# Kernel optimization log

Hardware: AMD Instinct MI355X
Metric: run time of the kernel (lower is better)

## Reference

```python
import jax, jax.numpy as jnp
import numpy as np

WINDOW = 8  # outlier_fraction = 0.125 -> 1 fp column kept per 8-wide window

# XnorBinaryLinear's STEBinary: sign in fwd, identity (straight-through) in bwd
@jax.custom_vjp
def ste_sign(x):
    return jnp.sign(x)

def _ste_fwd(x):
    return jnp.sign(x), None

def _ste_bwd(_, g):
    return (g,)

ste_sign.defvjp(_ste_fwd, _ste_bwd)


def quant_weight(w):
    # XnorBinaryLinear.quant_weight: per-row mean-center, sign, rescale by
    # detached per-row mean absolute value
    mu = jnp.mean(w, axis=-1, keepdims=True)
    wc = w - mu
    scale = jax.lax.stop_gradient(jnp.mean(jnp.abs(wc), axis=-1, keepdims=True))
    return ste_sign(wc) * scale


def binarize_except_outliers(w):
    # Binarize weight, then restore the max-|w| element of each flat 8-wide
    # window to full precision (calibration = argmax of |w| per window,
    # identical to outlier_calibration with L1 metric on first forward).
    wq = quant_weight(w)
    wv = w.reshape(-1, WINDOW)             # [n_windows, 8]
    idx = jnp.argmax(jnp.abs(wv), axis=1)  # [n_windows] outlier column per window
    mask = jnp.arange(WINDOW)[None, :] == idx[:, None]  # one-hot bool mask
    out = jnp.where(mask, wv, wq.reshape(-1, WINDOW))
    return out.reshape(w.shape)


def setup_inputs() -> dict:
    key = jax.random.key(0)
    k1, k2, k3 = jax.random.split(key, 3)
    x = jax.random.normal(k1, (4, 2048, 4096), dtype=jnp.float32)
    weight = jax.random.normal(k2, (4096, 4096), dtype=jnp.float32) * 0.02
    bias = jax.random.normal(k3, (4096,), dtype=jnp.float32) * 0.02
    return {"x": x, "weight": weight, "bias": bias}


def reference(x, weight, bias):
    w = binarize_except_outliers(weight)     # [OC, IC]
    return jnp.einsum('bsi,oi->bso', x, w) + bias
```

## Files before the change

kernel.cpp:

```cpp
#include <hip/hip_runtime.h>
#include <stdint.h>

#define M_DIM 8192
#define N_DIM 4096
#define K_DIM 4096

#define BM 128
#define BN 256
#define BK 64

typedef float v16f __attribute__((ext_vector_type(16)));
typedef __bf16 v8bf __attribute__((ext_vector_type(8)));

typedef __attribute__((address_space(3))) uint32_t lds_u32_t;
typedef const __attribute__((address_space(1))) uint32_t glb_u32_t;

__device__ inline uint16_t f2bf(float f) {
    union { float f; uint32_t u; } v; v.f = f;
    uint32_t r = v.u + 0x7fffu + ((v.u >> 16) & 1u);
    return (uint16_t)(r >> 16);
}

__global__ __launch_bounds__(256) void cvt_x(const float* __restrict__ x,
                                             uint16_t* __restrict__ xb,
                                             long long n8) {
    long long i = (long long)blockIdx.x * 256 + threadIdx.x;
    if (i >= n8) return;
    const float4* x4 = (const float4*)x;
    float4 a = x4[2 * i];
    float4 b = x4[2 * i + 1];
    union { uint16_t h[8]; uint4 u; } o;
    o.h[0] = f2bf(a.x); o.h[1] = f2bf(a.y); o.h[2] = f2bf(a.z); o.h[3] = f2bf(a.w);
    o.h[4] = f2bf(b.x); o.h[5] = f2bf(b.y); o.h[6] = f2bf(b.z); o.h[7] = f2bf(b.w);
    ((uint4*)xb)[i] = o.u;
}

__global__ __launch_bounds__(256) void make_weff(const float* __restrict__ w,
                                                 uint16_t* __restrict__ weff) {
    __shared__ double red[4];
    int row  = blockIdx.x;
    int tid  = threadIdx.x;
    int lane = tid & 63;
    int wid  = tid >> 6;

    const float* wr = w + (size_t)row * K_DIM;
    const float4* w4 = (const float4*)wr + tid * 4;
    float4 r0 = w4[0], r1 = w4[1], r2 = w4[2], r3 = w4[3];
    float v[16] = { r0.x, r0.y, r0.z, r0.w, r1.x, r1.y, r1.z, r1.w,
                    r2.x, r2.y, r2.z, r2.w, r3.x, r3.y, r3.z, r3.w };

    double s = 0.0;
#pragma unroll
    for (int j = 0; j < 16; j++) s += (double)v[j];
#pragma unroll
    for (int off = 32; off > 0; off >>= 1) s += __shfl_down(s, off);
    if (lane == 0) red[wid] = s;
    __syncthreads();
    double mu = (red[0] + red[1] + red[2] + red[3]) * (1.0 / 4096.0);
    __syncthreads();

    double sa = 0.0;
#pragma unroll
    for (int j = 0; j < 16; j++) sa += fabs((double)v[j] - mu);
#pragma unroll
    for (int off = 32; off > 0; off >>= 1) sa += __shfl_down(sa, off);
    if (lane == 0) red[wid] = sa;
    __syncthreads();
    double scale = (red[0] + red[1] + red[2] + red[3]) * (1.0 / 4096.0);

    float scf = (float)scale;
    union { uint16_t h[16]; uint4 u[2]; } o;
#pragma unroll
    for (int w2 = 0; w2 < 2; w2++) {
        int base = w2 * 8;
        int amax = 0;
        float mx = fabsf(v[base]);
#pragma unroll
        for (int j = 1; j < 8; j++) {
            float aj = fabsf(v[base + j]);
            if (aj > mx) { mx = aj; amax = j; }
        }
#pragma unroll
        for (int j = 0; j < 8; j++) {
            double wc = (double)v[base + j] - mu;
            float q = (wc > 0.0) ? scf : ((wc < 0.0) ? -scf : 0.0f);
            o.h[base + j] = f2bf((j == amax) ? v[base + j] : q);
        }
    }
    uint4* dst = (uint4*)(weff + (size_t)row * K_DIM + (size_t)tid * 16);
    dst[0] = o.u[0];
    dst[1] = o.u[1];
}

__device__ inline void async_cp16(const uint16_t* g, uint16_t* lds_uniform) {
    __builtin_amdgcn_global_load_lds((glb_u32_t*)g, (lds_u32_t*)lds_uniform, 16, 0, 0);
}

__global__ __launch_bounds__(256, 2) void gemm_bt(const uint16_t* __restrict__ A,
                                                  const uint16_t* __restrict__ B,
                                                  const float* __restrict__ bias,
                                                  float* __restrict__ C) {
    __shared__ __attribute__((aligned(16))) uint16_t As[BM * BK];
    __shared__ __attribute__((aligned(16))) uint16_t Bs[BN * BK];

    int tid  = threadIdx.x;
    int lane = tid & 63;
    int wid  = tid >> 6;
    int wm   = wid >> 1;
    int wn   = wid & 1;
    int half = lane >> 5;
    int ml   = lane & 31;

    long long bm = (long long)blockIdx.y * BM;
    long long bn = (long long)blockIdx.x * BN;

    v16f acc[2][4];
#pragma unroll
    for (int t = 0; t < 2; t++)
#pragma unroll
        for (int u = 0; u < 4; u++) acc[t][u] = (v16f)(0.0f);

    const uint16_t* Ab = A + (size_t)bm * K_DIM;
    const uint16_t* Bb = B + (size_t)bn * K_DIM;

    int lrow = lane >> 3;
    int cg   = (lane & 7) ^ lrow;

    for (int k0 = 0; k0 < K_DIM; k0 += BK) {
#pragma unroll
        for (int q = 0; q < 4; q++) {
            int ib = wid * 4 + q;
            int r  = ib * 8 + lrow;
            async_cp16(Ab + (size_t)r * K_DIM + k0 + cg * 8, As + ib * 512);
        }
#pragma unroll
        for (int q = 0; q < 8; q++) {
            int ib = wid * 8 + q;
            int r  = ib * 8 + lrow;
            async_cp16(Bb + (size_t)r * K_DIM + k0 + cg * 8, Bs + ib * 512);
        }
        __syncthreads();

#pragma unroll
        for (int s = 0; s < 4; s++) {
            int cc = s * 2 + half;
            v8bf af[2], bfv[4];
#pragma unroll
            for (int t = 0; t < 2; t++) {
                int r = wm * 64 + t * 32 + ml;
                af[t] = *(const v8bf*)&As[r * BK + ((cc ^ (r & 7)) * 8)];
            }
#pragma unroll
            for (int u = 0; u < 4; u++) {
                int r = wn * 128 + u * 32 + ml;
                bfv[u] = *(const v8bf*)&Bs[r * BK + ((cc ^ (r & 7)) * 8)];
            }
#pragma unroll
            for (int t = 0; t < 2; t++)
#pragma unroll
                for (int u = 0; u < 4; u++)
                    acc[t][u] = __builtin_amdgcn_mfma_f32_32x32x16_bf16(af[t], bfv[u], acc[t][u], 0, 0, 0);
        }
        __syncthreads();
    }

#pragma unroll
    for (int u = 0; u < 4; u++) {
        int n = (int)bn + wn * 128 + u * 32 + ml;
        float bj = bias[n];
#pragma unroll
        for (int t = 0; t < 2; t++) {
            int mb = (int)bm + wm * 64 + t * 32 + half * 4;
#pragma unroll
            for (int g = 0; g < 4; g++) {
#pragma unroll
                for (int d = 0; d < 4; d++) {
                    int row = mb + g * 8 + d;
                    C[(size_t)row * N_DIM + n] = acc[t][u][g * 4 + d] + bj;
                }
            }
        }
    }
}

extern "C" void kernel_launch(void* const* d_in, const int* in_sizes, int n_in,
                              void* d_out, int out_size, void* d_ws, size_t ws_size,
                              hipStream_t stream) {
    const float* x    = (const float*)d_in[0];
    const float* w    = (const float*)d_in[1];
    const float* bias = (const float*)d_in[2];
    float* out = (float*)d_out;

    uint16_t* xb   = (uint16_t*)d_ws;
    uint16_t* weff = (uint16_t*)((char*)d_ws + (size_t)M_DIM * K_DIM * 2);

    long long n8 = (long long)M_DIM * K_DIM / 8;
    cvt_x<<<dim3((unsigned)((n8 + 255) / 256)), dim3(256), 0, stream>>>(x, xb, n8);
    make_weff<<<dim3(N_DIM), dim3(256), 0, stream>>>(w, weff);
    gemm_bt<<<dim3(N_DIM / BN, M_DIM / BM), dim3(256), 0, stream>>>(xb, weff, bias, out);
}
```

Measured before the change: 512.8 us.

## Rewrite GEMM as 256x256 double-buffered pipelined kernel with 16x16 MFMA and block swizzle

Replaces the single-buffered 128x256 GEMM with a 512-thread, 256x256-tile kernel. It double-buffers LDS by K half-tiles and interleaves async global-to-LDS prefetch with MFMA phases, using explicit vmcnt waits, s_setprio and sched barriers. It also switches to 16x16x32 bf16 MFMA, adds a block-index swizzle for L2 locality, and turns the conversion kernel into a grid-stride loop over float4. The aim is to hide global load latency and raise MFMA utilization, at the cost of heavier register and LDS pressure and tricky hand-tuned wait counts.

```diff
diff --git a/kernel.cpp b/kernel.cpp
--- a/kernel.cpp
+++ b/kernel.cpp
@@ -5,11 +5,12 @@
 #define N_DIM 4096
 #define K_DIM 4096
 
-#define BM 128
+#define BM 256
 #define BN 256
 #define BK 64
-
-typedef float v16f __attribute__((ext_vector_type(16)));
+#define NT (K_DIM / BK)
+
+typedef float v4f __attribute__((ext_vector_type(4)));
 typedef __bf16 v8bf __attribute__((ext_vector_type(8)));
 
 typedef __attribute__((address_space(3))) uint32_t lds_u32_t;
@@ -23,16 +24,14 @@
 
 __global__ __launch_bounds__(256) void cvt_x(const float* __restrict__ x,
                                              uint16_t* __restrict__ xb,
-                                             long long n8) {
-    long long i = (long long)blockIdx.x * 256 + threadIdx.x;
-    if (i >= n8) return;
-    const float4* x4 = (const float4*)x;
-    float4 a = x4[2 * i];
-    float4 b = x4[2 * i + 1];
-    union { uint16_t h[8]; uint4 u; } o;
-    o.h[0] = f2bf(a.x); o.h[1] = f2bf(a.y); o.h[2] = f2bf(a.z); o.h[3] = f2bf(a.w);
-    o.h[4] = f2bf(b.x); o.h[5] = f2bf(b.y); o.h[6] = f2bf(b.z); o.h[7] = f2bf(b.w);
-    ((uint4*)xb)[i] = o.u;
+                                             long long n4) {
+    long long stride = (long long)gridDim.x * 256;
+    for (long long i = (long long)blockIdx.x * 256 + threadIdx.x; i < n4; i += stride) {
+        float4 a = ((const float4*)x)[i];
+        union { uint16_t h[4]; uint2 u; } o;
+        o.h[0] = f2bf(a.x); o.h[1] = f2bf(a.y); o.h[2] = f2bf(a.z); o.h[3] = f2bf(a.w);
+        ((uint2*)xb)[i] = o.u;
+    }
 }
 
 __global__ __launch_bounds__(256) void make_weff(const float* __restrict__ w,
@@ -92,93 +91,134 @@
     dst[1] = o.u[1];
 }
 
+
 __device__ inline void async_cp16(const uint16_t* g, uint16_t* lds_uniform) {
     __builtin_amdgcn_global_load_lds((glb_u32_t*)g, (lds_u32_t*)lds_uniform, 16, 0, 0);
 }
 
-__global__ __launch_bounds__(256, 2) void gemm_bt(const uint16_t* __restrict__ A,
+__device__ __forceinline__ void load4(v8bf (&d)[4], const uint16_t* base) {
+#pragma unroll
+    for (int i = 0; i < 4; ++i) d[i] = *(const v8bf*)(base + i * 512);
+}
+
+template<int MH>
+__device__ __forceinline__ void mfma16(v4f (&acc)[8][4], const v8bf (&a)[4], const v8bf (&b)[4]) {
+#pragma unroll
+    for (int fm = 0; fm < 4; ++fm)
+#pragma unroll
+        for (int fn = 0; fn < 4; ++fn)
+            acc[MH * 4 + fm][fn] =
+                __builtin_amdgcn_mfma_f32_16x16x32_bf16(a[fm], b[fn], acc[MH * 4 + fm][fn], 0, 0, 0);
+}
+
+#define SB   __builtin_amdgcn_sched_barrier(0)
+#define BAR  __builtin_amdgcn_s_barrier()
+#define PRIO1 __builtin_amdgcn_s_setprio(1)
+#define PRIO0 __builtin_amdgcn_s_setprio(0)
+#define VMWAIT(N) asm volatile("s_waitcnt vmcnt(" #N ")" ::: "memory")
+#define NOPW ((void)0)
+
+#define STG_A(BUFV, KHV, KOFF) do { \
+    async_cp16(a_s0 + (KOFF) + (KHV) * 32, ldsA + ((BUFV) * 2 + (KHV)) * 8192 + wid * 1024);       \
+    async_cp16(a_s1 + (KOFF) + (KHV) * 32, ldsA + ((BUFV) * 2 + (KHV)) * 8192 + wid * 1024 + 512); \
+} while (0)
+#define STG_B(BUFV, KHV, KOFF) do { \
+    async_cp16(b_s0 + (KOFF) + (KHV) * 32, ldsB + ((BUFV) * 2 + (KHV)) * 8192 + wid * 1024);       \
+    async_cp16(b_s1 + (KOFF) + (KHV) * 32, ldsB + ((BUFV) * 2 + (KHV)) * 8192 + wid * 1024 + 512); \
+} while (0)
+
+#define TILE(BUFV, PF1, PF2, WQ1, WQ3, KN1, KN2)                               \
+  {                                                                            \
+    v8bf a_f[4], b0[4], b1[4];                                                 \
+                                                            \
+    load4(a_f, rdA + ((BUFV) * 2 + 0) * 8192 + 0 * 2048);                      \
+    load4(b0,  rdB + ((BUFV) * 2 + 0) * 8192);                                 \
+    if (PF1) { STG_A(1 - (BUFV), 1, KN1); }                                    \
+    SB; BAR; SB;                                                               \
+    PRIO1; mfma16<0>(acc, a_f, b0); PRIO0;                                     \
+    SB; BAR;                                                                   \
+                                                            \
+    load4(a_f, rdA + ((BUFV) * 2 + 0) * 8192 + 1 * 2048);                      \
+    if (PF1) { STG_B(1 - (BUFV), 1, KN1); }                                    \
+    WQ1; SB; BAR; SB;                                                          \
+    PRIO1; mfma16<1>(acc, a_f, b0); PRIO0;                                     \
+    SB; BAR;                                                                   \
+                                                            \
+    load4(a_f, rdA + ((BUFV) * 2 + 1) * 8192 + 1 * 2048);                      \
+    load4(b1,  rdB + ((BUFV) * 2 + 1) * 8192);                                 \
+    if (PF2) { STG_A((BUFV), 0, KN2); }                                        \
+    SB; BAR; SB;                                                               \
+    PRIO1; mfma16<1>(acc, a_f, b1); PRIO0;                                     \
+    SB; BAR;                                                                   \
+                                                            \
+    load4(a_f, rdA + ((BUFV) * 2 + 1) * 8192 + 0 * 2048);                      \
+    if (PF2) { STG_B((BUFV), 0, KN2); }                                        \
+    WQ3; SB; BAR; SB;                                                          \
+    PRIO1; mfma16<0>(acc, a_f, b1); PRIO0;                                     \
+    SB; BAR;                                                                   \
+  }
+
+__global__ __launch_bounds__(512, 2) void gemm_bt(const uint16_t* __restrict__ A,
                                                   const uint16_t* __restrict__ B,
                                                   const float* __restrict__ bias,
                                                   float* __restrict__ C) {
-    __shared__ __attribute__((aligned(16))) uint16_t As[BM * BK];
-    __shared__ __attribute__((aligned(16))) uint16_t Bs[BN * BK];
+    __shared__ __attribute__((aligned(128))) uint16_t ldsA[4 * 8192];
+    __shared__ __attribute__((aligned(128))) uint16_t ldsB[4 * 8192];
 
     int tid  = threadIdx.x;
     int lane = tid & 63;
     int wid  = tid >> 6;
-    int wm   = wid >> 1;
-    int wn   = wid & 1;
-    int half = lane >> 5;
-    int ml   = lane & 31;
-
-    long long bm = (long long)blockIdx.y * BM;
-    long long bn = (long long)blockIdx.x * BN;
-
-    v16f acc[2][4];
-#pragma unroll
-    for (int t = 0; t < 2; t++)
-#pragma unroll
-        for (int u = 0; u < 4; u++) acc[t][u] = (v16f)(0.0f);
-
-    const uint16_t* Ab = A + (size_t)bm * K_DIM;
-    const uint16_t* Bb = B + (size_t)bn * K_DIM;
-
-    int lrow = lane >> 3;
-    int cg   = (lane & 7) ^ lrow;
-
-    for (int k0 = 0; k0 < K_DIM; k0 += BK) {
-#pragma unroll
-        for (int q = 0; q < 4; q++) {
-            int ib = wid * 4 + q;
-            int r  = ib * 8 + lrow;
-            async_cp16(Ab + (size_t)r * K_DIM + k0 + cg * 8, As + ib * 512);
-        }
-#pragma unroll
-        for (int q = 0; q < 8; q++) {
-            int ib = wid * 8 + q;
-            int r  = ib * 8 + lrow;
-            async_cp16(Bb + (size_t)r * K_DIM + k0 + cg * 8, Bs + ib * 512);
-        }
-        __syncthreads();
-
-#pragma unroll
-        for (int s = 0; s < 4; s++) {
-            int cc = s * 2 + half;
-            v8bf af[2], bfv[4];
-#pragma unroll
-            for (int t = 0; t < 2; t++) {
-                int r = wm * 64 + t * 32 + ml;
-                af[t] = *(const v8bf*)&As[r * BK + ((cc ^ (r & 7)) * 8)];
-            }
-#pragma unroll
-            for (int u = 0; u < 4; u++) {
-                int r = wn * 128 + u * 32 + ml;
-                bfv[u] = *(const v8bf*)&Bs[r * BK + ((cc ^ (r & 7)) * 8)];
-            }
-#pragma unroll
-            for (int t = 0; t < 2; t++)
-#pragma unroll
-                for (int u = 0; u < 4; u++)
-                    acc[t][u] = __builtin_amdgcn_mfma_f32_32x32x16_bf16(af[t], bfv[u], acc[t][u], 0, 0, 0);
-        }
-        __syncthreads();
-    }
-
-#pragma unroll
-    for (int u = 0; u < 4; u++) {
-        int n = (int)bn + wn * 128 + u * 32 + ml;
+    int wm   = wid >> 2;
+    int wn   = wid & 3;
+
+    int bid = blockIdx.x;
+    int swz = (bid & 7) * 64 + (bid >> 3);
+    long long bm = (long long)(swz >> 4) * BM;
+    long long bn = (long long)(swz & 15) * BN;
+
+    int srow = lane >> 2;
+    int scs  = (lane & 3) ^ ((srow >> 1) & 3);
+    const uint16_t* a_s0 = A + (size_t)(bm + wid * 32 +  0 + srow) * K_DIM + scs * 8;
+    const uint16_t* a_s1 = A + (size_t)(bm + wid * 32 + 16 + srow) * K_DIM + scs * 8;
+    const uint16_t* b_s0 = B + (size_t)(bn + wid * 32 +  0 + srow) * K_DIM + scs * 8;
+    const uint16_t* b_s1 = B + (size_t)(bn + wid * 32 + 16 + srow) * K_DIM + scs * 8;
+
+    int rl   = lane & 15;
+    int aoff = rl * 32 + (((lane >> 4) ^ ((rl >> 1) & 3)) * 8);
+    const uint16_t* rdA = ldsA + wm * 4096 + aoff;
+    const uint16_t* rdB = ldsB + wn * 2048 + aoff;
+
+    v4f acc[8][4];
+#pragma unroll
+    for (int i = 0; i < 8; ++i)
+#pragma unroll
+        for (int j = 0; j < 4; ++j) acc[i][j] = (v4f)(0.0f);
+
+    STG_A(0, 0, 0); STG_B(0, 0, 0); STG_A(0, 1, 0); STG_B(0, 1, 0);
+    STG_A(1, 0, 64); STG_B(1, 0, 64);
+    VMWAIT(8); SB; BAR;
+
+#pragma clang loop unroll(disable)
+    for (int it = 0; it < NT / 2 - 1; ++it) {
+        int t2 = it * 2;
+        TILE(0, 1, 1, VMWAIT(8), VMWAIT(8), (t2 + 1) * 64, (t2 + 2) * 64);
+        TILE(1, 1, 1, VMWAIT(8), VMWAIT(8), (t2 + 2) * 64, (t2 + 3) * 64);
+    }
+    TILE(0, 1, 0, VMWAIT(8), VMWAIT(4), (NT - 1) * 64, 0);
+    TILE(1, 0, 0, VMWAIT(0), NOPW, 0, 0);
+
+    int cl = lane & 15;
+    int ch = lane >> 4;
+#pragma unroll
+    for (int fn = 0; fn < 4; ++fn) {
+        int n = (int)bn + wn * 64 + fn * 16 + cl;
         float bj = bias[n];
 #pragma unroll
-        for (int t = 0; t < 2; t++) {
-            int mb = (int)bm + wm * 64 + t * 32 + half * 4;
-#pragma unroll
-            for (int g = 0; g < 4; g++) {
-#pragma unroll
-                for (int d = 0; d < 4; d++) {
-                    int row = mb + g * 8 + d;
-                    C[(size_t)row * N_DIM + n] = acc[t][u][g * 4 + d] + bj;
-                }
-            }
+        for (int m8 = 0; m8 < 8; ++m8) {
+            size_t rbase = (size_t)(bm + wm * 128 + m8 * 16 + ch * 4) * N_DIM + n;
+#pragma unroll
+            for (int g = 0; g < 4; ++g)
+                C[rbase + (size_t)g * N_DIM] = acc[m8][fn][g] + bj;
         }
     }
 }
@@ -194,8 +234,8 @@
     uint16_t* xb   = (uint16_t*)d_ws;
     uint16_t* weff = (uint16_t*)((char*)d_ws + (size_t)M_DIM * K_DIM * 2);
 
-    long long n8 = (long long)M_DIM * K_DIM / 8;
-    cvt_x<<<dim3((unsigned)((n8 + 255) / 256)), dim3(256), 0, stream>>>(x, xb, n8);
+    long long n4 = (long long)M_DIM * K_DIM / 4;
+    cvt_x<<<dim3(4096), dim3(256), 0, stream>>>(x, xb, n4);
     make_weff<<<dim3(N_DIM), dim3(256), 0, stream>>>(w, weff);
-    gemm_bt<<<dim3(N_DIM / BN, M_DIM / BM), dim3(256), 0, stream>>>(xb, weff, bias, out);
-}
+    gemm_bt<<<dim3(N_DIM / BN * (M_DIM / BM)), dim3(512), 0, stream>>>(xb, weff, bias, out);
+}
```

Result: slower. 536.8 us (+4.7%).
